# Kernel optimization log

Measured on AMD Instinct MI355X. Metric: run time of the kernel, lower is better.

The kernel has to match this reference:

```python
import jax, jax.numpy as jnp
import numpy as np

B, N, D_IN, H, R = 4096, 32, 256, 256, 3
VIRTUAL_DECAY = 0.7


def setup_inputs() -> dict:
    key = jax.random.key(0)
    ks = jax.random.split(key, 16)
    def xavier(k, shape):
        fan_in, fan_out = shape[-1], shape[-2]
        lim = np.sqrt(6.0 / (fan_in + fan_out))
        return jax.random.uniform(k, shape, jnp.float32, -lim, lim)
    return {
        'input_vec': jax.random.normal(ks[0], (B, D_IN), jnp.float32),
        'child_h': jax.random.normal(ks[1], (B, N, H), jnp.float32),
        'child_c': jax.random.normal(ks[2], (B, N, H), jnp.float32),
        'relation_ids': jax.random.randint(ks[3], (B, N), 0, R, jnp.int32),
        'virtual_mask': jax.random.randint(ks[4], (B, N), 0, 2, jnp.int32).astype(bool),
        'rel_emb': xavier(ks[5], (R, H)),
        'W_i': xavier(ks[6], (H, D_IN + H)), 'b_i': jnp.full((H,), 0.1, jnp.float32),
        'W_f': xavier(ks[7], (R, H, H)),     'b_f': jnp.full((R, H), 0.1, jnp.float32),
        'W_o': xavier(ks[8], (H, D_IN + H)), 'b_o': jnp.full((H,), 0.1, jnp.float32),
        'W_u': xavier(ks[9], (H, D_IN + H)), 'b_u': jnp.full((H,), 0.1, jnp.float32),
        'w_att': xavier(ks[10], (1, H)).reshape(H), 'b_att': jnp.full((1,), 0.1, jnp.float32),
    }


def reference(input_vec, child_h, child_c, relation_ids, virtual_mask,
              rel_emb, W_i, b_i, W_f, b_f, W_o, b_o, W_u, b_u, w_att, b_att):
    # virtual-node decay applied to both child states
    decay = jnp.where(virtual_mask, VIRTUAL_DECAY, 1.0)[..., None]          # (B,N,1)
    ch = child_h * decay                                                     # (B,N,H)
    cc = child_c * decay                                                     # (B,N,H)

    # relation-aware attention over children (softmax over child axis)
    re = rel_emb[relation_ids]                                               # (B,N,H)
    scores = jnp.einsum('bnh,h->bn', re + ch, w_att) + b_att[0]              # (B,N)
    attn = jax.nn.softmax(scores, axis=1)[..., None]                         # (B,N,1)
    child_h_sum = jnp.sum(ch * attn, axis=1)                                 # (B,H)

    # relation-routed forget gates: compute all R linears, gather by relation id
    # NOTE: original applies NO sigmoid to f (faithful to source)
    f_all = jnp.einsum('bnh,rgh->bnrg', ch, W_f) + b_f                       # (B,N,R,H)
    f = jnp.take_along_axis(f_all, relation_ids[:, :, None, None], axis=2)[:, :, 0, :]  # (B,N,H)
    child_c_sum = jnp.sum(f * cc, axis=1)                                    # (B,H)

    combined = jnp.concatenate([input_vec, child_h_sum], axis=-1)            # (B,D_IN+H)
    i = jax.nn.sigmoid(combined @ W_i.T + b_i)
    o = jax.nn.sigmoid(combined @ W_o.T + b_o)
    u = jnp.tanh(combined @ W_u.T + b_u)
    c = i * u + child_c_sum
    h = o * jnp.tanh(c)
    return (h, c)
```

## Files before the change

kernel.cpp:

```cpp
#include <hip/hip_runtime.h>
#include <hip/hip_bf16.h>
#include <math.h>


#define B_    4096
#define N_    32
#define H_    256
#define DIN_  256
#define R_    3
#define MB    8
#define NBC   2
#define CHUNKS (MB / NBC)
#define DECAY 0.7f

#define WS_WF   0
#define WS_WI   196608
#define WS_WO   327680
#define WS_WU   458752
#define WS_ELEMS 589824

typedef __bf16 bf16;
typedef bf16  bf16x8 __attribute__((ext_vector_type(8)));
typedef float f32x4  __attribute__((ext_vector_type(4)));

__device__ __forceinline__ float sigmoidf_(float x) { return 1.0f / (1.0f + __expf(-x)); }

__device__ __forceinline__ bf16x8 cvt8_nt(const float* p) {
    f32x4 a = __builtin_nontemporal_load((const f32x4*)p);
    f32x4 b = __builtin_nontemporal_load((const f32x4*)(p + 4));
    bf16x8 r;
    #pragma unroll
    for (int j = 0; j < 4; ++j) { r[j] = (bf16)a[j]; r[j + 4] = (bf16)b[j]; }
    return r;
}
__device__ __forceinline__ bf16x8 cvt8_c(const float* p) {
    f32x4 a = *(const f32x4*)p;
    f32x4 b = *(const f32x4*)(p + 4);
    bf16x8 r;
    #pragma unroll
    for (int j = 0; j < 4; ++j) { r[j] = (bf16)a[j]; r[j + 4] = (bf16)b[j]; }
    return r;
}

template<bool WSW>
__device__ __forceinline__ bf16x8 ldw8(const bf16* wsp, const float* fp, int idx) {
    if constexpr (WSW) return *(const bf16x8*)(wsp + idx);
    else               return cvt8_c(fp + idx);
}

__global__ __launch_bounds__(256) void wprep(
    const float* __restrict__ Wf, const float* __restrict__ Wi,
    const float* __restrict__ Wo, const float* __restrict__ Wu,
    bf16* __restrict__ ws)
{
    int i = (blockIdx.x * 256 + threadIdx.x) * 8;
    const float* src; int off;
    if      (i < WS_WI) { src = Wf; off = i - WS_WF; }
    else if (i < WS_WO) { src = Wi; off = i - WS_WI; }
    else if (i < WS_WU) { src = Wo; off = i - WS_WO; }
    else                { src = Wu; off = i - WS_WU; }
    *(bf16x8*)(ws + i) = cvt8_c(src + off);
}

template<bool WSW>
__global__ __launch_bounds__(512, 4) void fused_main(
    const float* __restrict__ ivec,
    const float* __restrict__ child_h, const float* __restrict__ child_c,
    const int*  __restrict__ rel_ids,  const void* __restrict__ vmaskp,
    const float* __restrict__ rel_emb,
    const float* __restrict__ W_i, const float* __restrict__ b_i,
    const float* __restrict__ W_f, const float* __restrict__ b_f,
    const float* __restrict__ W_o, const float* __restrict__ b_o,
    const float* __restrict__ W_u, const float* __restrict__ b_u,
    const float* __restrict__ w_att, const float* __restrict__ b_att,
    const bf16* __restrict__ ws, float* __restrict__ out)
{
    __shared__ __align__(16) bf16 chs[NBC][N_][264];
    __shared__ __align__(16) bf16 hsumL[MB][264];
    __shared__ float csL[MB][H_];
    __shared__ float watt[H_];
    __shared__ float bfl[R_][H_];
    __shared__ float dall[MB][N_];
    __shared__ int   rids[MB][N_];
    __shared__ float scoreT[NBC][N_];
    __shared__ float attnd[NBC][N_];
    __shared__ float rdotL[4];
    __shared__ int   m8flag;

    const int tid  = threadIdx.x;
    const int wave = tid >> 6;
    const int lane = tid & 63;
    const int t    = lane & 15;
    const int q    = lane >> 4;
    const int b0   = blockIdx.x * MB;

    const bf16* wfb = ws + WS_WF;
    const bf16* wib = ws + WS_WI;
    const bf16* wob = ws + WS_WO;
    const bf16* wub = ws + WS_WU;

    if (tid < 64) {
        const unsigned char* vb = (const unsigned char*)vmaskp;
        int bad = vb[tid * 4 + 1] | vb[tid * 4 + 2] | vb[tid * 4 + 3];
        unsigned long long any = __ballot(bad != 0);
        if (tid == 0) m8flag = (any != 0ull) ? 1 : 0;
    }
    __syncthreads();

    if (tid < 256) {
        watt[tid] = w_att[tid];
        int idx = b0 * N_ + tid;
        rids[tid >> 5][tid & 31] = rel_ids[idx];
        bool vm = m8flag ? (((const unsigned char*)vmaskp)[idx] != 0)
                         : (((const int*)vmaskp)[idx] != 0);
        dall[tid >> 5][tid & 31] = vm ? DECAY : 1.0f;
    }
    for (int i = tid; i < R_ * H_; i += 512) ((float*)bfl)[i] = b_f[i];
    if (tid == 0) rdotL[3] = b_att[0];
    __syncthreads();

    if (wave < R_) {
        int r = wave;
        float p = 0.f;
        #pragma unroll
        for (int j = 0; j < 4; ++j) {
            int h = lane * 4 + j;
            p += rel_emb[r * H_ + h] * watt[h];
        }
        #pragma unroll
        for (int off = 32; off >= 1; off >>= 1) p += __shfl_xor(p, off);
        if (lane == 0) rdotL[r] = p;
    }

    for (int ck = 0; ck < CHUNKS; ++ck) {
        __syncthreads();

        {
            size_t base = (size_t)(b0 + ck * NBC) * (N_ * H_);
            #pragma unroll
            for (int it = 0; it < 4; ++it) {
                int ge = (it * 512 + tid) << 3;
                int bi = ge >> 13, n = (ge >> 8) & 31, h = ge & 255;
                *(bf16x8*)(&chs[bi][n][h]) = cvt8_nt(child_h + base + ge);
            }
        }
        __syncthreads();

        {
            int pair = tid >> 3, part = tid & 7;
            int bi = pair >> 5, n = pair & 31;
            const bf16* row = chs[bi][n];
            float p = 0.f;
            #pragma unroll
            for (int jj = 0; jj < 4; ++jj) {
                bf16x8 v = *(const bf16x8*)(&row[part * 32 + jj * 8]);
                #pragma unroll
                for (int j = 0; j < 8; ++j) p += (float)v[j] * watt[part * 32 + jj * 8 + j];
            }
            p += __shfl_xor(p, 1);
            p += __shfl_xor(p, 2);
            p += __shfl_xor(p, 4);
            if (part == 0) scoreT[bi][n] = p;
        }
        __syncthreads();

        if (tid < NBC * N_) {
            int bi = tid >> 5, n = tid & 31;
            int bl = ck * NBC + bi;
            float d = dall[bl][n];
            float s = d * scoreT[bi][n] + rdotL[rids[bl][n]] + rdotL[3];
            float m = s;
            #pragma unroll
            for (int off = 16; off >= 1; off >>= 1) m = fmaxf(m, __shfl_xor(m, off));
            float e = __expf(s - m);
            float sum = e;
            #pragma unroll
            for (int off = 16; off >= 1; off >>= 1) sum += __shfl_xor(sum, off);
            attnd[bi][n] = (e / sum) * d;
        }
        __syncthreads();

        {
            int bi = tid >> 8, g = tid & 255;
            int bl = ck * NBC + bi;
            float s = 0.f;
            #pragma unroll 8
            for (int n = 0; n < N_; ++n) s += attnd[bi][n] * (float)chs[bi][n][g];
            hsumL[bl][g] = (bf16)s;
        }

        f32x4 acc[2][4];
        #pragma unroll
        for (int i = 0; i < 2; ++i)
            #pragma unroll
            for (int j = 0; j < 4; ++j)
                #pragma unroll
                for (int c = 0; c < 4; ++c) acc[i][j][c] = 0.0f;

        bf16x8 bzero;
        #pragma unroll
        for (int i = 0; i < 8; ++i) bzero[i] = (bf16)0.0f;

        int myrid[4];
        #pragma unroll
        for (int nt = 0; nt < 4; ++nt)
            myrid[nt] = rids[ck * NBC + (nt >> 1)][((nt & 1) << 4) + t];

        #pragma unroll
        for (int kc = 0; kc < 8; ++kc) {
            const int k = kc * 32 + q * 8;
            bf16x8 v[4];
            #pragma unroll
            for (int nt = 0; nt < 4; ++nt)
                v[nt] = *(const bf16x8*)(&chs[nt >> 1][((nt & 1) << 4) + t][k]);
            #pragma unroll
            for (int r = 0; r < R_; ++r) {
                bf16x8 afrag[2];
                #pragma unroll
                for (int m2 = 0; m2 < 2; ++m2) {
                    int g = (wave * 2 + m2) * 16 + t;
                    afrag[m2] = ldw8<WSW>(wfb, W_f, (r * H_ + g) * H_ + k);
                }
                #pragma unroll
                for (int nt = 0; nt < 4; ++nt) {
                    bf16x8 vm = (myrid[nt] == r) ? v[nt] : bzero;
                    acc[0][nt] = __builtin_amdgcn_mfma_f32_16x16x32_bf16(afrag[0], vm, acc[0][nt], 0, 0, 0);
                    acc[1][nt] = __builtin_amdgcn_mfma_f32_16x16x32_bf16(afrag[1], vm, acc[1][nt], 0, 0, 0);
                }
            }
        }
        __syncthreads();

        {
            size_t base = (size_t)(b0 + ck * NBC) * (N_ * H_);
            #pragma unroll
            for (int it = 0; it < 4; ++it) {
                int ge = (it * 512 + tid) << 3;
                int bi = ge >> 13, n = (ge >> 8) & 31, h = ge & 255;
                *(bf16x8*)(&chs[bi][n][h]) = cvt8_nt(child_c + base + ge);
            }
        }
        __syncthreads();

        #pragma unroll
        for (int m2 = 0; m2 < 2; ++m2) {
            #pragma unroll
            for (int reg = 0; reg < 4; ++reg) {
                const int g = (wave * 2 + m2) * 16 + q * 4 + reg;
                #pragma unroll
                for (int bi = 0; bi < NBC; ++bi) {
                    int bl = ck * NBC + bi;
                    float p = 0.f;
                    #pragma unroll
                    for (int j = 0; j < 2; ++j) {
                        int nt = bi * 2 + j;
                        int n  = (j << 4) + t;
                        float Q   = acc[m2][nt][reg];
                        float d   = dall[bl][n];
                        float ccv = (float)chs[bi][n][g];
                        float bfv = bfl[rids[bl][n]][g];
                        p += ccv * d * fmaf(d, Q, bfv);
                    }
                    p += __shfl_xor(p, 1);
                    p += __shfl_xor(p, 2);
                    p += __shfl_xor(p, 4);
                    p += __shfl_xor(p, 8);
                    if (t == 0) csL[bl][g] = p;
                }
            }
        }
    }
    __syncthreads();

    const int j0 = wave * 32;
    const int tt = t & 7;
    f32x4 accI[2], accO[2], accU[2];
    #pragma unroll
    for (int c = 0; c < 2; ++c)
        #pragma unroll
        for (int r = 0; r < 4; ++r) { accI[c][r] = 0.f; accO[c][r] = 0.f; accU[c][r] = 0.f; }

    #pragma unroll
    for (int kc = 0; kc < 16; ++kc) {
        const int k = kc * 32 + q * 8;
        bf16x8 a;
        if (kc < 8) a = cvt8_nt(ivec + (size_t)(b0 + tt) * DIN_ + k);
        else        a = *(const bf16x8*)(&hsumL[tt][k - 256]);
        #pragma unroll
        for (int c = 0; c < 2; ++c) {
            int j = j0 + c * 16 + t;
            bf16x8 bI = ldw8<WSW>(wib, W_i, j * 512 + k);
            bf16x8 bO = ldw8<WSW>(wob, W_o, j * 512 + k);
            bf16x8 bU = ldw8<WSW>(wub, W_u, j * 512 + k);
            accI[c] = __builtin_amdgcn_mfma_f32_16x16x32_bf16(a, bI, accI[c], 0, 0, 0);
            accO[c] = __builtin_amdgcn_mfma_f32_16x16x32_bf16(a, bO, accO[c], 0, 0, 0);
            accU[c] = __builtin_amdgcn_mfma_f32_16x16x32_bf16(a, bU, accU[c], 0, 0, 0);
        }
    }

    if (q < 2) {
        #pragma unroll
        for (int c = 0; c < 2; ++c) {
            const int j = j0 + c * 16 + t;
            float biv = b_i[j], bov = b_o[j], buv = b_u[j];
            #pragma unroll
            for (int reg = 0; reg < 4; ++reg) {
                int bl = q * 4 + reg;
                size_t o1 = (size_t)(b0 + bl) * H_ + j;
                size_t o2 = (size_t)B_ * H_ + o1;
                float iv = sigmoidf_(accI[c][reg] + biv);
                float ov = sigmoidf_(accO[c][reg] + bov);
                float uv = tanhf(accU[c][reg] + buv);
                float cv = fmaf(iv, uv, csL[bl][j]);
                float hv = ov * tanhf(cv);
                __builtin_nontemporal_store(hv, out + o1);
                __builtin_nontemporal_store(cv, out + o2);
            }
        }
    }
}

extern "C" void kernel_launch(void* const* d_in, const int* in_sizes, int n_in,
                              void* d_out, int out_size, void* d_ws, size_t ws_size,
                              hipStream_t stream)
{
    const float* ivec    = (const float*)d_in[0];
    const float* child_h = (const float*)d_in[1];
    const float* child_c = (const float*)d_in[2];
    const int*   relids  = (const int*)d_in[3];
    const void*  vmask   = d_in[4];
    const float* rel_emb = (const float*)d_in[5];
    const float* W_i     = (const float*)d_in[6];
    const float* b_i     = (const float*)d_in[7];
    const float* W_f     = (const float*)d_in[8];
    const float* b_f     = (const float*)d_in[9];
    const float* W_o     = (const float*)d_in[10];
    const float* b_o     = (const float*)d_in[11];
    const float* W_u     = (const float*)d_in[12];
    const float* b_u     = (const float*)d_in[13];
    const float* w_att   = (const float*)d_in[14];
    const float* b_att   = (const float*)d_in[15];
    float* out = (float*)d_out;
    bf16*  ws  = (bf16*)d_ws;

    const bool wsw = (ws_size >= (size_t)WS_ELEMS * sizeof(bf16));

    if (wsw) {
        hipLaunchKernelGGL(wprep, dim3(WS_ELEMS / 8 / 256), dim3(256), 0, stream,
                           W_f, W_i, W_o, W_u, ws);
        hipLaunchKernelGGL((fused_main<true>), dim3(B_ / MB), dim3(512), 0, stream,
                           ivec, child_h, child_c, relids, vmask, rel_emb,
                           W_i, b_i, W_f, b_f, W_o, b_o, W_u, b_u, w_att, b_att,
                           ws, out);
    } else {
        hipLaunchKernelGGL((fused_main<false>), dim3(B_ / MB), dim3(512), 0, stream,
                           ivec, child_h, child_c, relids, vmask, rel_emb,
                           W_i, b_i, W_f, b_f, W_o, b_o, W_u, b_u, w_att, b_att,
                           ws, out);
    }
}
```

Baseline: 458.9 us.

## Halve batch per block, fuse score dot into load, read child_c directly from global

Each block now handles 4 batch rows, one per chunk, instead of 8 rows in chunks of 2. This shrinks the shared memory footprint and accumulator registers, and the launch bounds ask for 8 blocks per CU instead of 4. The attention score dot product is computed while child_h is being converted to bf16, which removes a separate pass and a barrier. child_c is loaded straight from global into registers in the MFMA output layout rather than staged through LDS. The cost is that every weight fragment is now reused across half as many batch rows, so weight traffic per output doubles.

```diff
diff --git a/kernel.cpp b/kernel.cpp
--- a/kernel.cpp
+++ b/kernel.cpp
@@ -8,9 +8,8 @@
 #define H_    256
 #define DIN_  256
 #define R_    3
-#define MB    8
-#define NBC   2
-#define CHUNKS (MB / NBC)
+#define MB    4
+#define CHUNKS MB
 #define DECAY 0.7f
 
 #define WS_WF   0
@@ -63,7 +62,7 @@
 }
 
 template<bool WSW>
-__global__ __launch_bounds__(512, 4) void fused_main(
+__global__ __launch_bounds__(512, 8) void fused_main(
     const float* __restrict__ ivec,
     const float* __restrict__ child_h, const float* __restrict__ child_c,
     const int*  __restrict__ rel_ids,  const void* __restrict__ vmaskp,
@@ -75,15 +74,15 @@
     const float* __restrict__ w_att, const float* __restrict__ b_att,
     const bf16* __restrict__ ws, float* __restrict__ out)
 {
-    __shared__ __align__(16) bf16 chs[NBC][N_][264];
+    __shared__ __align__(16) bf16 chs[N_][264];
     __shared__ __align__(16) bf16 hsumL[MB][264];
     __shared__ float csL[MB][H_];
     __shared__ float watt[H_];
     __shared__ float bfl[R_][H_];
     __shared__ float dall[MB][N_];
     __shared__ int   rids[MB][N_];
-    __shared__ float scoreT[NBC][N_];
-    __shared__ float attnd[NBC][N_];
+    __shared__ float scoreT[N_];
+    __shared__ float attnd[N_];
     __shared__ float rdotL[4];
     __shared__ int   m8flag;
 
@@ -107,8 +106,8 @@
     }
     __syncthreads();
 
-    if (tid < 256) {
-        watt[tid] = w_att[tid];
+    if (tid < H_) watt[tid] = w_att[tid];
+    if (tid < MB * N_) {
         int idx = b0 * N_ + tid;
         rids[tid >> 5][tid & 31] = rel_ids[idx];
         bool vm = m8flag ? (((const unsigned char*)vmaskp)[idx] != 0)
@@ -136,39 +135,39 @@
         __syncthreads();
 
         {
-            size_t base = (size_t)(b0 + ck * NBC) * (N_ * H_);
-            #pragma unroll
-            for (int it = 0; it < 4; ++it) {
+            size_t base = (size_t)(b0 + ck) * (N_ * H_);
+            float dp0, dp1;
+            #pragma unroll
+            for (int it = 0; it < 2; ++it) {
                 int ge = (it * 512 + tid) << 3;
-                int bi = ge >> 13, n = (ge >> 8) & 31, h = ge & 255;
-                *(bf16x8*)(&chs[bi][n][h]) = cvt8_nt(child_h + base + ge);
+                int n = ge >> 8, h = ge & 255;
+                f32x4 a = __builtin_nontemporal_load((const f32x4*)(child_h + base + ge));
+                f32x4 b = __builtin_nontemporal_load((const f32x4*)(child_h + base + ge + 4));
+                bf16x8 r; float p = 0.f;
+                #pragma unroll
+                for (int j = 0; j < 4; ++j) {
+                    r[j] = (bf16)a[j]; r[j + 4] = (bf16)b[j];
+                    p += a[j] * watt[h + j] + b[j] * watt[h + 4 + j];
+                }
+                *(bf16x8*)(&chs[n][h]) = r;
+                if (it == 0) dp0 = p; else dp1 = p;
+            }
+            #pragma unroll
+            for (int off = 16; off >= 1; off >>= 1) {
+                dp0 += __shfl_xor(dp0, off);
+                dp1 += __shfl_xor(dp1, off);
+            }
+            if ((tid & 31) == 0) {
+                scoreT[tid >> 5] = dp0;
+                scoreT[16 + (tid >> 5)] = dp1;
             }
         }
         __syncthreads();
 
-        {
-            int pair = tid >> 3, part = tid & 7;
-            int bi = pair >> 5, n = pair & 31;
-            const bf16* row = chs[bi][n];
-            float p = 0.f;
-            #pragma unroll
-            for (int jj = 0; jj < 4; ++jj) {
-                bf16x8 v = *(const bf16x8*)(&row[part * 32 + jj * 8]);
-                #pragma unroll
-                for (int j = 0; j < 8; ++j) p += (float)v[j] * watt[part * 32 + jj * 8 + j];
-            }
-            p += __shfl_xor(p, 1);
-            p += __shfl_xor(p, 2);
-            p += __shfl_xor(p, 4);
-            if (part == 0) scoreT[bi][n] = p;
-        }
-        __syncthreads();
-
-        if (tid < NBC * N_) {
-            int bi = tid >> 5, n = tid & 31;
-            int bl = ck * NBC + bi;
-            float d = dall[bl][n];
-            float s = d * scoreT[bi][n] + rdotL[rids[bl][n]] + rdotL[3];
+        if (tid < N_) {
+            int n = tid;
+            float d = dall[ck][n];
+            float s = d * scoreT[n] + rdotL[rids[ck][n]] + rdotL[3];
             float m = s;
             #pragma unroll
             for (int off = 16; off >= 1; off >>= 1) m = fmaxf(m, __shfl_xor(m, off));
@@ -176,24 +175,23 @@
             float sum = e;
             #pragma unroll
             for (int off = 16; off >= 1; off >>= 1) sum += __shfl_xor(sum, off);
-            attnd[bi][n] = (e / sum) * d;
+            attnd[n] = (e / sum) * d;
         }
         __syncthreads();
 
-        {
-            int bi = tid >> 8, g = tid & 255;
-            int bl = ck * NBC + bi;
+        if (tid < H_) {
+            int g = tid;
             float s = 0.f;
             #pragma unroll 8
-            for (int n = 0; n < N_; ++n) s += attnd[bi][n] * (float)chs[bi][n][g];
-            hsumL[bl][g] = (bf16)s;
-        }
-
-        f32x4 acc[2][4];
+            for (int n = 0; n < N_; ++n) s += attnd[n] * (float)chs[n][g];
+            hsumL[ck][g] = (bf16)s;
+        }
+
+        f32x4 acc[2][2];
         #pragma unroll
         for (int i = 0; i < 2; ++i)
             #pragma unroll
-            for (int j = 0; j < 4; ++j)
+            for (int j = 0; j < 2; ++j)
                 #pragma unroll
                 for (int c = 0; c < 4; ++c) acc[i][j][c] = 0.0f;
 
@@ -201,71 +199,62 @@
         #pragma unroll
         for (int i = 0; i < 8; ++i) bzero[i] = (bf16)0.0f;
 
-        int myrid[4];
-        #pragma unroll
-        for (int nt = 0; nt < 4; ++nt)
-            myrid[nt] = rids[ck * NBC + (nt >> 1)][((nt & 1) << 4) + t];
+        int myrid[2];
+        #pragma unroll
+        for (int j = 0; j < 2; ++j)
+            myrid[j] = rids[ck][(j << 4) + t];
 
         #pragma unroll
         for (int kc = 0; kc < 8; ++kc) {
             const int k = kc * 32 + q * 8;
-            bf16x8 v[4];
-            #pragma unroll
-            for (int nt = 0; nt < 4; ++nt)
-                v[nt] = *(const bf16x8*)(&chs[nt >> 1][((nt & 1) << 4) + t][k]);
+            bf16x8 v[2];
+            #pragma unroll
+            for (int j = 0; j < 2; ++j)
+                v[j] = *(const bf16x8*)(&chs[(j << 4) + t][k]);
             #pragma unroll
             for (int r = 0; r < R_; ++r) {
                 bf16x8 afrag[2];
                 #pragma unroll
                 for (int m2 = 0; m2 < 2; ++m2) {
-                    int g = (wave * 2 + m2) * 16 + t;
+                    int g = wave * 32 + m2 * 16 + t;
                     afrag[m2] = ldw8<WSW>(wfb, W_f, (r * H_ + g) * H_ + k);
                 }
                 #pragma unroll
-                for (int nt = 0; nt < 4; ++nt) {
-                    bf16x8 vm = (myrid[nt] == r) ? v[nt] : bzero;
-                    acc[0][nt] = __builtin_amdgcn_mfma_f32_16x16x32_bf16(afrag[0], vm, acc[0][nt], 0, 0, 0);
-                    acc[1][nt] = __builtin_amdgcn_mfma_f32_16x16x32_bf16(afrag[1], vm, acc[1][nt], 0, 0, 0);
+                for (int j = 0; j < 2; ++j) {
+                    bf16x8 vm = (myrid[j] == r) ? v[j] : bzero;
+                    acc[0][j] = __builtin_amdgcn_mfma_f32_16x16x32_bf16(afrag[0], vm, acc[0][j], 0, 0, 0);
+                    acc[1][j] = __builtin_amdgcn_mfma_f32_16x16x32_bf16(afrag[1], vm, acc[1][j], 0, 0, 0);
                 }
             }
         }
-        __syncthreads();
 
         {
-            size_t base = (size_t)(b0 + ck * NBC) * (N_ * H_);
-            #pragma unroll
-            for (int it = 0; it < 4; ++it) {
-                int ge = (it * 512 + tid) << 3;
-                int bi = ge >> 13, n = (ge >> 8) & 31, h = ge & 255;
-                *(bf16x8*)(&chs[bi][n][h]) = cvt8_nt(child_c + base + ge);
-            }
-        }
-        __syncthreads();
-
-        #pragma unroll
-        for (int m2 = 0; m2 < 2; ++m2) {
-            #pragma unroll
-            for (int reg = 0; reg < 4; ++reg) {
-                const int g = (wave * 2 + m2) * 16 + q * 4 + reg;
-                #pragma unroll
-                for (int bi = 0; bi < NBC; ++bi) {
-                    int bl = ck * NBC + bi;
+            size_t cbase = (size_t)(b0 + ck) * (N_ * H_);
+            f32x4 cc[2][2];
+            #pragma unroll
+            for (int m2 = 0; m2 < 2; ++m2)
+                #pragma unroll
+                for (int j = 0; j < 2; ++j)
+                    cc[m2][j] = __builtin_nontemporal_load(
+                        (const f32x4*)(child_c + cbase + ((j << 4) + t) * H_
+                                       + wave * 32 + m2 * 16 + q * 4));
+            #pragma unroll
+            for (int m2 = 0; m2 < 2; ++m2) {
+                #pragma unroll
+                for (int reg = 0; reg < 4; ++reg) {
+                    const int g = wave * 32 + m2 * 16 + q * 4 + reg;
                     float p = 0.f;
                     #pragma unroll
                     for (int j = 0; j < 2; ++j) {
-                        int nt = bi * 2 + j;
-                        int n  = (j << 4) + t;
-                        float Q   = acc[m2][nt][reg];
-                        float d   = dall[bl][n];
-                        float ccv = (float)chs[bi][n][g];
-                        float bfv = bfl[rids[bl][n]][g];
-                        p += ccv * d * fmaf(d, Q, bfv);
+                        int n = (j << 4) + t;
+                        float d = dall[ck][n];
+                        p += cc[m2][j][reg] * d * fmaf(d, acc[m2][j][reg], bfl[rids[ck][n]][g]);
                     }
                     p += __shfl_xor(p, 1);
                     p += __shfl_xor(p, 2);
                     p += __shfl_xor(p, 4);
                     p += __shfl_xor(p, 8);
-                    if (t == 0) csL[bl][g] = p;
+                    if (t == 0) csL[ck][g] = p;
                 }
             }
         }
@@ -273,7 +262,7 @@
     __syncthreads();
 
     const int j0 = wave * 32;
-    const int tt = t & 7;
+    const int tt = t & 3;
     f32x4 accI[2], accO[2], accU[2];
     #pragma unroll
     for (int c = 0; c < 2; ++c)
@@ -298,14 +287,14 @@
         }
     }
 
-    if (q < 2) {
+    if (q == 0) {
         #pragma unroll
         for (int c = 0; c < 2; ++c) {
             const int j = j0 + c * 16 + t;
             float biv = b_i[j], bov = b_o[j], buv = b_u[j];
             #pragma unroll
             for (int reg = 0; reg < 4; ++reg) {
-                int bl = q * 4 + reg;
+                int bl = reg;
                 size_t o1 = (size_t)(b0 + bl) * H_ + j;
                 size_t o2 = (size_t)B_ * H_ + o1;
                 float iv = sigmoidf_(accI[c][reg] + biv);
```

After: 747.5 us. 62.9% more time.

## Fuse score dot into load, shuffle-broadcast softmax, read child_c straight into registers

Applied to the files above, without the earlier changes.

The attention score dot product is now computed in fp32 while child_h is loaded and converted, which drops the separate LDS score pass. Every wave computes the softmax redundantly and hands attention weights to the weighted sum through lane shuffles, so the attnd shared array and its barriers go away. child_c is no longer staged in LDS: each lane loads the values it needs in MFMA layout directly from global memory, which removes two more block barriers per chunk. In exchange the child_c reads are uncoalesced, each only 16 bytes per lane, and every wave repeats the softmax work.

```diff
diff --git a/kernel.cpp b/kernel.cpp
--- a/kernel.cpp
+++ b/kernel.cpp
@@ -82,8 +82,7 @@
     __shared__ float bfl[R_][H_];
     __shared__ float dall[MB][N_];
     __shared__ int   rids[MB][N_];
-    __shared__ float scoreT[NBC][N_];
-    __shared__ float attnd[NBC][N_];
+    __shared__ float scoreT[NBC * N_];
     __shared__ float rdotL[4];
     __shared__ int   m8flag;
 
@@ -137,38 +136,44 @@
 
         {
             size_t base = (size_t)(b0 + ck * NBC) * (N_ * H_);
+            float dp[4];
             #pragma unroll
             for (int it = 0; it < 4; ++it) {
                 int ge = (it * 512 + tid) << 3;
-                int bi = ge >> 13, n = (ge >> 8) & 31, h = ge & 255;
-                *(bf16x8*)(&chs[bi][n][h]) = cvt8_nt(child_h + base + ge);
+                int row = ge >> 8;
+                int h = ge & 255;
+                f32x4 a = __builtin_nontemporal_load((const f32x4*)(child_h + base + ge));
+                f32x4 b = __builtin_nontemporal_load((const f32x4*)(child_h + base + ge + 4));
+                bf16x8 r; float p = 0.f;
+                #pragma unroll
+                for (int j = 0; j < 4; ++j) {
+                    r[j] = (bf16)a[j]; r[j + 4] = (bf16)b[j];
+                    p += a[j] * watt[h + j] + b[j] * watt[h + 4 + j];
+                }
+                *(bf16x8*)(&chs[row >> 5][row & 31][h]) = r;
+                dp[it] = p;
+            }
+            #pragma unroll
+            for (int off = 16; off >= 1; off >>= 1) {
+                dp[0] += __shfl_xor(dp[0], off);
+                dp[1] += __shfl_xor(dp[1], off);
+                dp[2] += __shfl_xor(dp[2], off);
+                dp[3] += __shfl_xor(dp[3], off);
+            }
+            if ((tid & 31) == 0) {
+                int grp = tid >> 5;
+                #pragma unroll
+                for (int it = 0; it < 4; ++it) scoreT[it * 16 + grp] = dp[it];
             }
         }
         __syncthreads();
 
+        float att;
         {
-            int pair = tid >> 3, part = tid & 7;
-            int bi = pair >> 5, n = pair & 31;
-            const bf16* row = chs[bi][n];
-            float p = 0.f;
-            #pragma unroll
-            for (int jj = 0; jj < 4; ++jj) {
-                bf16x8 v = *(const bf16x8*)(&row[part * 32 + jj * 8]);
-                #pragma unroll
-                for (int j = 0; j < 8; ++j) p += (float)v[j] * watt[part * 32 + jj * 8 + j];
-            }
-            p += __shfl_xor(p, 1);
-            p += __shfl_xor(p, 2);
-            p += __shfl_xor(p, 4);
-            if (part == 0) scoreT[bi][n] = p;
-        }
-        __syncthreads();
-
-        if (tid < NBC * N_) {
-            int bi = tid >> 5, n = tid & 31;
+            int bi = lane >> 5, n = lane & 31;
             int bl = ck * NBC + bi;
             float d = dall[bl][n];
-            float s = d * scoreT[bi][n] + rdotL[rids[bl][n]] + rdotL[3];
+            float s = d * scoreT[lane] + rdotL[rids[bl][n]] + rdotL[3];
             float m = s;
             #pragma unroll
             for (int off = 16; off >= 1; off >>= 1) m = fmaxf(m, __shfl_xor(m, off));
@@ -176,16 +181,18 @@
             float sum = e;
             #pragma unroll
             for (int off = 16; off >= 1; off >>= 1) sum += __shfl_xor(sum, off);
-            attnd[bi][n] = (e / sum) * d;
-        }
-        __syncthreads();
+            att = (e / sum) * d;
+        }
 
         {
             int bi = tid >> 8, g = tid & 255;
             int bl = ck * NBC + bi;
             float s = 0.f;
             #pragma unroll 8
-            for (int n = 0; n < N_; ++n) s += attnd[bi][n] * (float)chs[bi][n][g];
+            for (int n = 0; n < N_; ++n) {
+                float av = __shfl(att, (bi << 5) | n);
+                s += av * (float)chs[bi][n][g];
+            }
             hsumL[bl][g] = (bf16)s;
         }
 
@@ -229,43 +236,43 @@
                 }
             }
         }
-        __syncthreads();
 
         {
-            size_t base = (size_t)(b0 + ck * NBC) * (N_ * H_);
-            #pragma unroll
-            for (int it = 0; it < 4; ++it) {
-                int ge = (it * 512 + tid) << 3;
-                int bi = ge >> 13, n = (ge >> 8) & 31, h = ge & 255;
-                *(bf16x8*)(&chs[bi][n][h]) = cvt8_nt(child_c + base + ge);
-            }
-        }
-        __syncthreads();
-
-        #pragma unroll
-        for (int m2 = 0; m2 < 2; ++m2) {
-            #pragma unroll
-            for (int reg = 0; reg < 4; ++reg) {
-                const int g = (wave * 2 + m2) * 16 + q * 4 + reg;
+            f32x4 cc[2][2][2];
+            #pragma unroll
+            for (int m2 = 0; m2 < 2; ++m2)
                 #pragma unroll
                 for (int bi = 0; bi < NBC; ++bi) {
-                    int bl = ck * NBC + bi;
-                    float p = 0.f;
+                    size_t cbase = (size_t)(b0 + ck * NBC + bi) * (N_ * H_);
                     #pragma unroll
-                    for (int j = 0; j < 2; ++j) {
-                        int nt = bi * 2 + j;
-                        int n  = (j << 4) + t;
-                        float Q   = acc[m2][nt][reg];
-                        float d   = dall[bl][n];
-                        float ccv = (float)chs[bi][n][g];
-                        float bfv = bfl[rids[bl][n]][g];
-                        p += ccv * d * fmaf(d, Q, bfv);
+                    for (int j = 0; j < 2; ++j)
+                        cc[m2][bi][j] = __builtin_nontemporal_load(
+                            (const f32x4*)(child_c + cbase + (size_t)(((j << 4) + t)) * H_
+                                           + (wave * 2 + m2) * 16 + q * 4));
+                }
+            #pragma unroll
+            for (int m2 = 0; m2 < 2; ++m2) {
+                #pragma unroll
+                for (int reg = 0; reg < 4; ++reg) {
+                    const int g = (wave * 2 + m2) * 16 + q * 4 + reg;
+                    #pragma unroll
+                    for (int bi = 0; bi < NBC; ++bi) {
+                        int bl = ck * NBC + bi;
+                        float p = 0.f;
+                        #pragma unroll
+                        for (int j = 0; j < 2; ++j) {
+                            int nt = bi * 2 + j;
+                            int n  = (j << 4) + t;
+                            float d = dall[bl][n];
+                            p += cc[m2][bi][j][reg] * d
+                                 * fmaf(d, acc[m2][nt][reg], bfl[rids[bl][n]][g]);
+                        }
+                        p += __shfl_xor(p, 1);
+                        p += __shfl_xor(p, 2);
+                        p += __shfl_xor(p, 4);
+                        p += __shfl_xor(p, 8);
+                        if (t == 0) csL[bl][g] = p;
                     }
-                    p += __shfl_xor(p, 1);
-                    p += __shfl_xor(p, 2);
-                    p += __shfl_xor(p, 4);
-                    p += __shfl_xor(p, 8);
-                    if (t == 0) csL[bl][g] = p;
                 }
             }
         }
```

After: 461.7 us. About the same (+0.6%).
